# Performance work log

Measured on AMD Instinct MI355X. Metric: run time of the kernel, lower is better.

Reference implementation:

```python
import jax, jax.numpy as jnp
import numpy as np

B, A, V, D = 16, 1024, 512, 512
TEMPERATURE = 1.0
NEG = jnp.float32(-1e30)  # stand-in for -inf (avoids inf-inf NaNs in grads)
EPS = 1e-12               # F.normalize eps


def setup_inputs() -> dict:
    key = jax.random.key(0)
    k1, k2, k3 = jax.random.split(key, 3)
    audio_features = jax.random.normal(k1, (B, A, D), jnp.float32)
    video_features = jax.random.normal(k2, (B, V, D), jnp.float32)
    W = jax.random.normal(k3, (D, D), jnp.float32) / np.sqrt(D)  # nn.Linear weight [out,in]
    b = jnp.zeros((D,), jnp.float32)
    return {"audio_features": audio_features, "video_features": video_features, "W": W, "b": b}


def _normalize(x):
    n = jnp.linalg.norm(x, axis=-1, keepdims=True)
    return x / jnp.maximum(n, EPS)


def _dtw_score(sim):
    # sim: [B, A, V]. dp[i,j] = sim[i-1,j-1] + max(dp[i-1,j], dp[i,j-1], dp[i-1,j-1]).
    Bn, An, Vn = sim.shape
    init_row = jnp.full((Bn, Vn + 1), NEG).at[:, 0].set(0.0)  # dp row 0

    def row_step(prev_row, cost_row):
        # prev_row: [B, V+1], cost_row: [B, V]
        def col_step(left, xs):
            c, up, diag = xs  # each [B]
            val = c + jnp.maximum(jnp.maximum(up, left), diag)
            return val, val

        xs = (cost_row.T, prev_row[:, 1:].T, prev_row[:, :-1].T)  # [V, B] each
        _, vals = jax.lax.scan(col_step, jnp.full((Bn,), NEG), xs)  # vals: [V, B]
        new_row = jnp.concatenate([jnp.full((Bn, 1), NEG), vals.T], axis=1)
        return new_row, None

    final_row, _ = jax.lax.scan(row_step, init_row, jnp.swapaxes(sim, 0, 1))
    return final_row[:, -1]  # dp[:, A, V]


def reference(audio_features, video_features, W, b):
    audio_proj = jnp.einsum('bad,ed->bae', audio_features, W) + b
    video_proj = jnp.einsum('bvd,ed->bve', video_features, W) + b
    a_n = _normalize(audio_proj)
    v_n = _normalize(video_proj)
    similarity = jnp.einsum('bad,bvd->bav', a_n, v_n) / TEMPERATURE  # [B, A, V]
    alignment_score = _dtw_score(similarity)                          # [B]
    path_prob = jax.nn.softmax(similarity, axis=-1)
    aligned_video = jnp.einsum('bav,bvd->bad', path_prob, video_features)  # [B, A, D]
    return aligned_video, alignment_score
```

## Files before the change

### kernel.cpp

```cpp
#include <hip/hip_runtime.h>
#include <math.h>

#define B_DIM 16
#define A_DIM 1024
#define V_DIM 512
#define D_DIM 512
#define NEGV  (-1e30f)
#define SKT_W 768

typedef short bf16x8 __attribute__((ext_vector_type(8)));
typedef float floatx4 __attribute__((ext_vector_type(4)));

__device__ __forceinline__ short bf16_rne(float f) {
    unsigned u = __float_as_uint(f);
    return (short)((u + 0x7fffu + ((u >> 16) & 1u)) >> 16);
}

__device__ __forceinline__ float max3f(float a, float b, float c) {
    float d;
    asm("v_max3_f32 %0, %1, %2, %3" : "=v"(d) : "v"(a), "v"(b), "v"(c));
    return d;
}

__global__ __launch_bounds__(256) void cvt3_bf16_kernel(
    const float* __restrict__ in0, unsigned short* __restrict__ out0, int nb0,
    const float* __restrict__ in1, unsigned short* __restrict__ out1, int nb1,
    const float* __restrict__ in2, unsigned short* __restrict__ out2)
{
    int blk = blockIdx.x;
    const float* in; unsigned short* out;
    if (blk < nb0)              { in = in0; out = out0; }
    else if (blk < nb0 + nb1)   { in = in1; out = out1; blk -= nb0; }
    else                        { in = in2; out = out2; blk -= nb0 + nb1; }
    const int i = blk * 256 + threadIdx.x;
    float4 u = ((const float4*)in)[2*i];
    float4 v = ((const float4*)in)[2*i + 1];
    bf16x8 h;
    h[0]=bf16_rne(u.x); h[1]=bf16_rne(u.y); h[2]=bf16_rne(u.z); h[3]=bf16_rne(u.w);
    h[4]=bf16_rne(v.x); h[5]=bf16_rne(v.y); h[6]=bf16_rne(v.z); h[7]=bf16_rne(v.w);
    *(bf16x8*)(out + (size_t)i * 8) = h;
}

__device__ __forceinline__ void gemm_tile_body(
    const unsigned short* __restrict__ Ab, const unsigned short* __restrict__ Bb,
    const float* __restrict__ bias, float* __restrict__ Cb,
    int m0, int n0, int K, int N, int tid,
    unsigned short* lA, unsigned short* lB)
{
    const int lane = tid & 63;
    const int w = tid >> 6, wy = w >> 1, wx = w & 1;

    const int u0 = tid, u1 = tid + 256;
    const int r_u0 = ((u0 >> 6) << 4) + (u0 & 15), k_u0 = ((u0 >> 4) & 3) * 8;
    const int r_u1 = ((u1 >> 6) << 4) + (u1 & 15), k_u1 = ((u1 >> 4) & 3) * 8;

    const unsigned short* gA0 = Ab + (size_t)(m0 + r_u0) * K + k_u0;
    const unsigned short* gA1 = Ab + (size_t)(m0 + r_u1) * K + k_u1;
    const unsigned short* gB0 = Bb + (size_t)(n0 + r_u0) * K + k_u0;
    const unsigned short* gB1 = Bb + (size_t)(n0 + r_u1) * K + k_u1;

    floatx4 acc[4][4];
    #pragma unroll
    for (int i = 0; i < 4; ++i)
        #pragma unroll
        for (int j = 0; j < 4; ++j) acc[i][j] = (floatx4){0.f, 0.f, 0.f, 0.f};

    bf16x8 a0 = *(const bf16x8*)(gA0);
    bf16x8 a1 = *(const bf16x8*)(gA1);
    bf16x8 b0 = *(const bf16x8*)(gB0);
    bf16x8 b1 = *(const bf16x8*)(gB1);

    for (int k0 = 0; k0 < K; k0 += 32) {
        __syncthreads();
        *(bf16x8*)&lA[(size_t)u0 * 8] = a0;
        *(bf16x8*)&lA[(size_t)u1 * 8] = a1;
        *(bf16x8*)&lB[(size_t)u0 * 8] = b0;
        *(bf16x8*)&lB[(size_t)u1 * 8] = b1;
        __syncthreads();

        if (k0 + 32 < K) {
            a0 = *(const bf16x8*)(gA0 + k0 + 32);
            a1 = *(const bf16x8*)(gA1 + k0 + 32);
            b0 = *(const bf16x8*)(gB0 + k0 + 32);
            b1 = *(const bf16x8*)(gB1 + k0 + 32);
        }

        bf16x8 fa[4], fb[4];
        #pragma unroll
        for (int t = 0; t < 4; ++t) {
            fa[t] = *(const bf16x8*)&lA[(((wy*4 + t)*64) + lane) * 8];
            fb[t] = *(const bf16x8*)&lB[(((wx*4 + t)*64) + lane) * 8];
        }
        #pragma unroll
        for (int i = 0; i < 4; ++i)
            #pragma unroll
            for (int j = 0; j < 4; ++j)
                acc[i][j] = __builtin_amdgcn_mfma_f32_16x16x32_bf16(fa[i], fb[j], acc[i][j], 0, 0, 0);
    }

    const int q = lane >> 4, c = lane & 15;
    #pragma unroll
    for (int i = 0; i < 4; ++i)
        #pragma unroll
        for (int j = 0; j < 4; ++j) {
            const int n = n0 + (wx*4 + j)*16 + c;
            const float bv = bias ? bias[n] : 0.f;
            #pragma unroll
            for (int r = 0; r < 4; ++r) {
                const int m = m0 + (wy*4 + i)*16 + q*4 + r;
                Cb[(size_t)m * N + n] = acc[i][j][r] + bv;
            }
        }
}

__global__ __launch_bounds__(256) void gemm_bf16_nt(
    const unsigned short* __restrict__ Ag, const unsigned short* __restrict__ Bg,
    const float* __restrict__ bias, float* __restrict__ Cg,
    int M, int N, int K, size_t strA, size_t strB, size_t strC)
{
    __shared__ __align__(16) unsigned short lA[8*64*8];
    __shared__ __align__(16) unsigned short lB[8*64*8];
    const unsigned short* Ab = Ag + (size_t)blockIdx.z * strA;
    const unsigned short* Bb = Bg + (size_t)blockIdx.z * strB;
    float*                Cb = Cg + (size_t)blockIdx.z * strC;
    gemm_tile_body(Ab, Bb, bias, Cb, blockIdx.y * 128, blockIdx.x * 128, K, N,
                   threadIdx.x, lA, lB);
}

__global__ __launch_bounds__(256) void gemm_proj2(
    const unsigned short* __restrict__ abf, const unsigned short* __restrict__ vbf,
    const unsigned short* __restrict__ Wbf, const float* __restrict__ bias,
    float* __restrict__ a_p, float* __restrict__ v_p)
{
    __shared__ __align__(16) unsigned short lA[8*64*8];
    __shared__ __align__(16) unsigned short lB[8*64*8];
    const int by = blockIdx.y;
    const unsigned short* Ab; float* Cb; int m0;
    if (by < 128) { Ab = abf; Cb = a_p; m0 = by * 128; }
    else          { Ab = vbf; Cb = v_p; m0 = (by - 128) * 128; }
    gemm_tile_body(Ab, Wbf, bias, Cb, m0, blockIdx.x * 128, D_DIM, D_DIM,
                   threadIdx.x, lA, lB);
}

__global__ __launch_bounds__(256) void norm2_transpose_kernel(
    const float* __restrict__ a_p, unsigned short* __restrict__ a_nb,
    const float* __restrict__ v_p, unsigned short* __restrict__ v_nb,
    const float* __restrict__ video, unsigned short* __restrict__ vTb)
{
    __shared__ float t[32][33];
    const int bx = blockIdx.x;
    if (bx < 6144) {
        const float* in; unsigned short* out; int rb;
        if (bx < 4096) { in = a_p; out = a_nb; rb = bx; }
        else           { in = v_p; out = v_nb; rb = bx - 4096; }
        const int wave = threadIdx.x >> 6;
        const int lane = threadIdx.x & 63;
        const size_t r = (size_t)rb * 4 + wave;
        const float* p = in + r * D_DIM + lane * 8;
        float4 u = *(const float4*)p;
        float4 w = *(const float4*)(p + 4);
        float ss = u.x*u.x + u.y*u.y + u.z*u.z + u.w*u.w
                 + w.x*w.x + w.y*w.y + w.z*w.z + w.w*w.w;
        #pragma unroll
        for (int m = 1; m < 64; m <<= 1) ss += __shfl_xor(ss, m, 64);
        const float inv = 1.0f / fmaxf(sqrtf(ss), 1e-12f);
        bf16x8 h;
        h[0]=bf16_rne(u.x*inv); h[1]=bf16_rne(u.y*inv); h[2]=bf16_rne(u.z*inv); h[3]=bf16_rne(u.w*inv);
        h[4]=bf16_rne(w.x*inv); h[5]=bf16_rne(w.y*inv); h[6]=bf16_rne(w.z*inv); h[7]=bf16_rne(w.w*inv);
        *(bf16x8*)(out + r * D_DIM + lane * 8) = h;
    } else {
        const int tt = bx - 6144;
        const int d0 = (tt & 15) * 32;
        const int v0 = ((tt >> 4) & 15) * 32;
        const int b  = tt >> 8;
        const int x = threadIdx.x & 31, y0 = (threadIdx.x >> 5) * 4;
        const float* I = video + ((size_t)b * V_DIM + v0) * D_DIM + d0;
        #pragma unroll
        for (int r = 0; r < 4; ++r) t[y0 + r][x] = I[(size_t)(y0 + r) * D_DIM + x];
        __syncthreads();
        unsigned short* O = vTb + ((size_t)b * D_DIM + d0) * V_DIM + v0;
        #pragma unroll
        for (int r = 0; r < 4; ++r) O[(size_t)(y0 + r) * V_DIM + x] = (unsigned short)bf16_rne(t[x][y0 + r]);
    }
}

template <int CTRL, int RMASK>
__device__ __forceinline__ float fdpp(float oldv, float src) {
    int r = __builtin_amdgcn_update_dpp(
        __float_as_int(oldv), __float_as_int(src), CTRL, RMASK, 0xF, false);
    return __int_as_float(r);
}

__global__ __launch_bounds__(256) void softmax_skewT_kernel(
    const float* __restrict__ sim, unsigned short* __restrict__ Pbf,
    float* __restrict__ skewT)
{
    __shared__ float tl[4][520];
    const int wave = threadIdx.x >> 6;
    const int lane = threadIdx.x & 63;
    const size_t r = (size_t)blockIdx.x * 4 + wave;
    const float* p = sim + r * V_DIM + lane * 8;
    float4 u = *(const float4*)p;
    float4 w = *(const float4*)(p + 4);
    float s[8] = {u.x,u.y,u.z,u.w,w.x,w.y,w.z,w.w};

    float m = s[0];
    #pragma unroll
    for (int k = 1; k < 8; ++k) m = fmaxf(m, s[k]);
    #pragma unroll
    for (int t = 1; t < 64; t <<= 1) m = fmaxf(m, __shfl_xor(m, t, 64));

    const float L2E = 1.44269504f;
    float ex[8];
    float e = 0.f;
    #pragma unroll
    for (int k = 0; k < 8; ++k) { ex[k] = exp2f((s[k] - m) * L2E); e += ex[k]; }
    #pragma unroll
    for (int t = 1; t < 64; t <<= 1) e += __shfl_xor(e, t, 64);
    const float ri = 1.0f / e;

    bf16x8 h;
    #pragma unroll
    for (int k = 0; k < 8; ++k) h[k] = bf16_rne(ex[k] * ri);
    *(bf16x8*)(Pbf + r * V_DIM + lane * 8) = h;

    #pragma unroll
    for (int k = 0; k < 8; ++k) tl[wave][lane * 8 + k] = s[k];
    __syncthreads();

    const int r0 = blockIdx.x * 4;
    const int b  = r0 >> 10;
    const int i0 = r0 & 1023;
    const int g  = i0 >> 2;
    const int off = (g & 63) + 80 * (g >> 6);
    float* sbase = skewT + (size_t)b * SKT_W * 1024 + i0;
    #pragma unroll
    for (int cc = 0; cc < 2; ++cc) {
        const int c = threadIdx.x + cc * 256;
        int pc = c + off; if (pc >= SKT_W) pc -= SKT_W;
        float4 v = make_float4(tl[0][c], tl[1][c], tl[2][c], tl[3][c]);
        *(float4*)(sbase + (size_t)pc * 1024) = v;
    }
}

__global__ __launch_bounds__(512) void pv_dtw_kernel(
    const unsigned short* __restrict__ Pbf, const unsigned short* __restrict__ vTb,
    const float* __restrict__ skewT, float* __restrict__ out_aligned,
    float* __restrict__ out_score)
{
    __shared__ __align__(16) unsigned short shmem_u16[16384];

    const int half = threadIdx.x >> 8;
    const int tid  = threadIdx.x & 255;

    if (blockIdx.x < 8) {
        const int b    = blockIdx.x * 2 + half;
        const int lane = tid & 63;
        const int wv   = tid >> 6;
        const int off  = lane + 80 * wv;

        float* bndAll = (float*)shmem_u16 + half * (3 * 528);
        float* bndP = bndAll + wv * 528;
        const float* bndC = bndAll + (wv > 0 ? wv - 1 : 0) * 528;
        for (int i = tid; i < 3 * 528; i += 256) bndAll[i] = NEGV;
        __syncthreads();

        const float* Sb = skewT + (size_t)b * SKT_W * 1024 + 4 * tid;

        float dp[4] = {NEGV, NEGV, NEGV, NEGV};
        float st[16];
        float upC = NEGV;
        float upL = (tid == 0) ? 0.0f : NEGV;

        float4 CA[8], CB[8], CC[8], CD[8];
        #pragma unroll
        for (int k = 0; k < 8; ++k) {
            CA[k] = *(const float4*)(Sb + (size_t)k * 1024);
            CB[k] = *(const float4*)(Sb + (size_t)(k + 8) * 1024);
            CC[k] = *(const float4*)(Sb + (size_t)(k + 16) * 1024);
            CD[k] = *(const float4*)(Sb + (size_t)(k + 24) * 1024);
        }

#define DTW_STEP(K, CK, FK)                                                   \
        {                                                                     \
            const unsigned jj = (unsigned)(sb + (K) - off);                   \
            if (jj < 512u) {                                                  \
                float u = upC, g = upL, old, nd;                              \
                old = dp[0]; nd = (CK).x + max3f(u, dp[0], g); dp[0] = nd; g = old; u = nd; \
                old = dp[1]; nd = (CK).y + max3f(u, dp[1], g); dp[1] = nd; g = old; u = nd; \
                old = dp[2]; nd = (CK).z + max3f(u, dp[2], g); dp[2] = nd; g = old; u = nd; \
                old = dp[3]; nd = (CK).w + max3f(u, dp[3], g); dp[3] = nd;                  \
            }                                                                 \
            st[K] = dp[3];                                                    \
            upL = upC;                                                        \
            upC = fdpp<0x138, 0xF>((FK), dp[3]);                              \
        }

#define DTW_BATCH16(P, Q)                                                     \
        {                                                                     \
            const int ps = sb + 8 - 80 * wv;                                  \
            float f[16];                                                      \
            _Pragma("unroll")                                                 \
            for (int k = 0; k < 16; ++k) {                                    \
                int idx = ps + k;                                             \
                idx = idx < 0 ? 0 : (idx > 527 ? 527 : idx);                  \
                f[k] = (wv > 0) ? bndC[idx] : NEGV;                           \
            }                                                                 \
            DTW_STEP(0,  P[0], f[0])  DTW_STEP(1,  P[1], f[1])                \
            DTW_STEP(2,  P[2], f[2])  DTW_STEP(3,  P[3], f[3])                \
            DTW_STEP(4,  P[4], f[4])  DTW_STEP(5,  P[5], f[5])                \
            DTW_STEP(6,  P[6], f[6])  DTW_STEP(7,  P[7], f[7])                \
            DTW_STEP(8,  Q[0], f[8])  DTW_STEP(9,  Q[1], f[9])                \
            DTW_STEP(10, Q[2], f[10]) DTW_STEP(11, Q[3], f[11])               \
            DTW_STEP(12, Q[4], f[12]) DTW_STEP(13, Q[5], f[13])               \
            DTW_STEP(14, Q[6], f[14]) DTW_STEP(15, Q[7], f[15])               \
            {                                                                 \
                _Pragma("unroll")                                             \
                for (int k = 0; k < 8; ++k) {                                 \
                    int c1 = sb + 32 + k; if (c1 >= SKT_W) c1 -= SKT_W;       \
                    P[k] = *(const float4*)(Sb + (size_t)c1 * 1024);          \
                    int c2 = sb + 40 + k; if (c2 >= SKT_W) c2 -= SKT_W;       \
                    Q[k] = *(const float4*)(Sb + (size_t)c2 * 1024);          \
                }                                                             \
            }                                                                 \
            if (wv < 3 && lane == 63) {                                       \
                _Pragma("unroll")                                             \
                for (int k = 0; k < 16; ++k) {                                \
                    const int jp = sb + k - 63 - 80 * wv;                     \
                    const int adr = ((unsigned)jp < 512u) ? (jp + 7) : 527;   \
                    bndP[adr] = st[k];                                        \
                }                                                             \
            }                                                                 \
            asm volatile("s_waitcnt lgkmcnt(0)" ::: "memory");                \
            __builtin_amdgcn_s_barrier();                                     \
            asm volatile("" ::: "memory");                                    \
        }

        #pragma unroll 1
        for (int bt = 0; bt < 52; bt += 2) {
            int sb = bt * 16;
            DTW_BATCH16(CA, CB)
            sb += 16;
            DTW_BATCH16(CC, CD)
        }
#undef DTW_BATCH16
#undef DTW_STEP
        if (tid == 255) out_score[b] = dp[3];
        return;
    }

    const int tile = (blockIdx.x - 8) * 2 + half;
    const int n0 = (tile & 3) * 128;
    const int m0 = ((tile >> 2) & 7) * 128;
    const int bz = tile >> 5;

    const unsigned short* Ab = Pbf + (size_t)bz * A_DIM * V_DIM;
    const unsigned short* Bb = vTb + (size_t)bz * V_DIM * D_DIM;
    float*                Cb = out_aligned + (size_t)bz * A_DIM * D_DIM;

    unsigned short* lA = shmem_u16 + half * 8192;
    unsigned short* lB = lA + 4096;
    gemm_tile_body(Ab, Bb, nullptr, Cb, m0, n0, V_DIM, D_DIM, tid, lA, lB);
}

extern "C" void kernel_launch(void* const* d_in, const int* in_sizes, int n_in,
                              void* d_out, int out_size, void* d_ws, size_t ws_size,
                              hipStream_t stream)
{
    const float* audio = (const float*)d_in[0];
    const float* video = (const float*)d_in[1];
    const float* W     = (const float*)d_in[2];
    const float* bias  = (const float*)d_in[3];

    float* out_aligned = (float*)d_out;
    float* out_score   = (float*)d_out + (size_t)B_DIM * A_DIM * D_DIM;

    const size_t NA = (size_t)B_DIM * A_DIM * D_DIM;
    const size_t NV = (size_t)B_DIM * V_DIM * D_DIM;
    const size_t NS = (size_t)B_DIM * A_DIM * V_DIM;

    float* ws = (float*)d_ws;
    float*          a_p  = ws;
    float*          v_p  = a_p + NA;
    float*          sim  = v_p + NV;
    unsigned short* abf  = (unsigned short*)(sim + NS);
    unsigned short* vbf  = (unsigned short*)(sim + NS) + NA;
    unsigned short* v_nb = vbf + NV;
    unsigned short* Wbf  = v_nb + NV;
    unsigned short* a_nb = abf;
    unsigned short* Pbf  = abf;
    unsigned short* vTb  = vbf;
    float*          skewT = a_p;

    {
        const int nb_a = (int)(NA / 8 / 256);
        const int nb_v = (int)(NV / 8 / 256);
        const int nb_w = D_DIM * D_DIM / 8 / 256;
        cvt3_bf16_kernel<<<dim3(nb_a + nb_v + nb_w), dim3(256), 0, stream>>>(
            audio, abf, nb_a, video, vbf, nb_v, W, Wbf);
    }

    gemm_proj2<<<dim3(D_DIM/128, 192), dim3(256), 0, stream>>>(
        abf, vbf, Wbf, bias, a_p, v_p);

    norm2_transpose_kernel<<<dim3(4096 + 2048 + 4096), dim3(256), 0, stream>>>(
        a_p, a_nb, v_p, v_nb, video, vTb);

    gemm_bf16_nt<<<dim3(V_DIM/128, A_DIM/128, B_DIM), dim3(256), 0, stream>>>(
        a_nb, v_nb, nullptr, sim, A_DIM, V_DIM, D_DIM,
        (size_t)A_DIM*D_DIM, (size_t)V_DIM*D_DIM, (size_t)A_DIM*V_DIM);

    softmax_skewT_kernel<<<dim3((B_DIM*A_DIM)/4), dim3(256), 0, stream>>>(sim, Pbf, skewT);

    pv_dtw_kernel<<<dim3(8 + 256), dim3(512), 0, stream>>>(
        Pbf, vTb, skewT, out_aligned, out_score);
}
```

Baseline: 329.0 us.

## Fuse bf16 conversion into projection GEMM, widen softmax-skew blocks, split pv/dtw blocks

Drops the separate fp32-to-bf16 conversion kernel. The projection GEMM now loads fp32 inputs directly and converts them with packed bf16 conversion instructions while staging into LDS, which removes one launch and a full round trip of the inputs through memory. The softmax/skew kernel now handles 16 rows per block, so it writes full 16-float runs of the skewed transpose, and it explicitly zero-fills padding columns. The pv/dtw kernel changes from 512-thread blocks, each holding two halves, to 256-thread blocks with one DTW or GEMM tile each. This may change occupancy and the overlap between the DTW chain and the GEMM tiles.

```diff
diff --git a/kernel.cpp b/kernel.cpp
--- a/kernel.cpp
+++ b/kernel.cpp
@@ -22,23 +22,13 @@
     return d;
 }
 
-__global__ __launch_bounds__(256) void cvt3_bf16_kernel(
-    const float* __restrict__ in0, unsigned short* __restrict__ out0, int nb0,
-    const float* __restrict__ in1, unsigned short* __restrict__ out1, int nb1,
-    const float* __restrict__ in2, unsigned short* __restrict__ out2)
-{
-    int blk = blockIdx.x;
-    const float* in; unsigned short* out;
-    if (blk < nb0)              { in = in0; out = out0; }
-    else if (blk < nb0 + nb1)   { in = in1; out = out1; blk -= nb0; }
-    else                        { in = in2; out = out2; blk -= nb0 + nb1; }
-    const int i = blk * 256 + threadIdx.x;
-    float4 u = ((const float4*)in)[2*i];
-    float4 v = ((const float4*)in)[2*i + 1];
-    bf16x8 h;
-    h[0]=bf16_rne(u.x); h[1]=bf16_rne(u.y); h[2]=bf16_rne(u.z); h[3]=bf16_rne(u.w);
-    h[4]=bf16_rne(v.x); h[5]=bf16_rne(v.y); h[6]=bf16_rne(v.z); h[7]=bf16_rne(v.w);
-    *(bf16x8*)(out + (size_t)i * 8) = h;
+__device__ __forceinline__ bf16x8 cvt8(float4 u, float4 w) {
+    union { unsigned int ui[4]; bf16x8 h; } r;
+    asm("v_cvt_pk_bf16_f32 %0, %1, %2" : "=v"(r.ui[0]) : "v"(u.x), "v"(u.y));
+    asm("v_cvt_pk_bf16_f32 %0, %1, %2" : "=v"(r.ui[1]) : "v"(u.z), "v"(u.w));
+    asm("v_cvt_pk_bf16_f32 %0, %1, %2" : "=v"(r.ui[2]) : "v"(w.x), "v"(w.y));
+    asm("v_cvt_pk_bf16_f32 %0, %1, %2" : "=v"(r.ui[3]) : "v"(w.z), "v"(w.w));
+    return r.h;
 }
 
 __device__ __forceinline__ void gemm_tile_body(
@@ -113,6 +103,78 @@
         }
 }
 
+__device__ __forceinline__ void gemm_tile_body_f32in(
+    const float* __restrict__ Ab, const float* __restrict__ Bb,
+    const float* __restrict__ bias, float* __restrict__ Cb,
+    int m0, int n0, int K, int N, int tid,
+    unsigned short* lA, unsigned short* lB)
+{
+    const int lane = tid & 63;
+    const int w = tid >> 6, wy = w >> 1, wx = w & 1;
+
+    const int u0 = tid, u1 = tid + 256;
+    const int r_u0 = ((u0 >> 6) << 4) + (u0 & 15), k_u0 = ((u0 >> 4) & 3) * 8;
+    const int r_u1 = ((u1 >> 6) << 4) + (u1 & 15), k_u1 = ((u1 >> 4) & 3) * 8;
+
+    const float* gA0 = Ab + (size_t)(m0 + r_u0) * K + k_u0;
+    const float* gA1 = Ab + (size_t)(m0 + r_u1) * K + k_u1;
+    const float* gB0 = Bb + (size_t)(n0 + r_u0) * K + k_u0;
+    const float* gB1 = Bb + (size_t)(n0 + r_u1) * K + k_u1;
+
+    floatx4 acc[4][4];
+    #pragma unroll
+    for (int i = 0; i < 4; ++i)
+        #pragma unroll
+        for (int j = 0; j < 4; ++j) acc[i][j] = (floatx4){0.f, 0.f, 0.f, 0.f};
+
+    float4 a0u = *(const float4*)(gA0), a0w = *(const float4*)(gA0 + 4);
+    float4 a1u = *(const float4*)(gA1), a1w = *(const float4*)(gA1 + 4);
+    float4 b0u = *(const float4*)(gB0), b0w = *(const float4*)(gB0 + 4);
+    float4 b1u = *(const float4*)(gB1), b1w = *(const float4*)(gB1 + 4);
+
+    for (int k0 = 0; k0 < K; k0 += 32) {
+        __syncthreads();
+        *(bf16x8*)&lA[(size_t)u0 * 8] = cvt8(a0u, a0w);
+        *(bf16x8*)&lA[(size_t)u1 * 8] = cvt8(a1u, a1w);
+        *(bf16x8*)&lB[(size_t)u0 * 8] = cvt8(b0u, b0w);
+        *(bf16x8*)&lB[(size_t)u1 * 8] = cvt8(b1u, b1w);
+        __syncthreads();
+
+        if (k0 + 32 < K) {
+            a0u = *(const float4*)(gA0 + k0 + 32); a0w = *(const float4*)(gA0 + k0 + 36);
+            a1u = *(const float4*)(gA1 + k0 + 32); a1w = *(const float4*)(gA1 + k0 + 36);
+            b0u = *(const float4*)(gB0 + k0 + 32); b0w = *(const float4*)(gB0 + k0 + 36);
+            b1u = *(const float4*)(gB1 + k0 + 32); b1w = *(const float4*)(gB1 + k0 + 36);
+        }
+
+        bf16x8 fa[4], fb[4];
+        #pragma unroll
+        for (int t = 0; t < 4; ++t) {
+            fa[t] = *(const bf16x8*)&lA[(((wy*4 + t)*64) + lane) * 8];
+            fb[t] = *(const bf16x8*)&lB[(((wx*4 + t)*64) + lane) * 8];
+        }
+        #pragma unroll
+        for (int i = 0; i < 4; ++i)
+            #pragma unroll
+            for (int j = 0; j < 4; ++j)
+                acc[i][j] = __builtin_amdgcn_mfma_f32_16x16x32_bf16(fa[i], fb[j], acc[i][j], 0, 0, 0);
+    }
+
+    const int q = lane >> 4, c = lane & 15;
+    #pragma unroll
+    for (int i = 0; i < 4; ++i)
+        #pragma unroll
+        for (int j = 0; j < 4; ++j) {
+            const int n = n0 + (wx*4 + j)*16 + c;
+            const float bv = bias ? bias[n] : 0.f;
+            #pragma unroll
+            for (int r = 0; r < 4; ++r) {
+                const int m = m0 + (wy*4 + i)*16 + q*4 + r;
+                Cb[(size_t)m * N + n] = acc[i][j][r] + bv;
+            }
+        }
+}
+
 __global__ __launch_bounds__(256) void gemm_bf16_nt(
     const unsigned short* __restrict__ Ag, const unsigned short* __restrict__ Bg,
     const float* __restrict__ bias, float* __restrict__ Cg,
@@ -127,19 +189,19 @@
                    threadIdx.x, lA, lB);
 }
 
-__global__ __launch_bounds__(256) void gemm_proj2(
-    const unsigned short* __restrict__ abf, const unsigned short* __restrict__ vbf,
-    const unsigned short* __restrict__ Wbf, const float* __restrict__ bias,
+__global__ __launch_bounds__(256) void gemm_proj2_f32(
+    const float* __restrict__ audio, const float* __restrict__ video,
+    const float* __restrict__ W, const float* __restrict__ bias,
     float* __restrict__ a_p, float* __restrict__ v_p)
 {
     __shared__ __align__(16) unsigned short lA[8*64*8];
     __shared__ __align__(16) unsigned short lB[8*64*8];
     const int by = blockIdx.y;
-    const unsigned short* Ab; float* Cb; int m0;
-    if (by < 128) { Ab = abf; Cb = a_p; m0 = by * 128; }
-    else          { Ab = vbf; Cb = v_p; m0 = (by - 128) * 128; }
-    gemm_tile_body(Ab, Wbf, bias, Cb, m0, blockIdx.x * 128, D_DIM, D_DIM,
-                   threadIdx.x, lA, lB);
+    const float* Ab; float* Cb; int m0;
+    if (by < 128) { Ab = audio; Cb = a_p; m0 = by * 128; }
+    else          { Ab = video; Cb = v_p; m0 = (by - 128) * 128; }
+    gemm_tile_body_f32in(Ab, W, bias, Cb, m0, blockIdx.x * 128, D_DIM, D_DIM,
+                         threadIdx.x, lA, lB);
 }
 
 __global__ __launch_bounds__(256) void norm2_transpose_kernel(
@@ -191,75 +253,81 @@
     return __int_as_float(r);
 }
 
-__global__ __launch_bounds__(256) void softmax_skewT_kernel(
+__global__ __launch_bounds__(256) void softmax_skewT16_kernel(
     const float* __restrict__ sim, unsigned short* __restrict__ Pbf,
     float* __restrict__ skewT)
 {
-    __shared__ float tl[4][520];
+    __shared__ float tl[16][512];
     const int wave = threadIdx.x >> 6;
     const int lane = threadIdx.x & 63;
-    const size_t r = (size_t)blockIdx.x * 4 + wave;
-    const float* p = sim + r * V_DIM + lane * 8;
-    float4 u = *(const float4*)p;
-    float4 w = *(const float4*)(p + 4);
-    float s[8] = {u.x,u.y,u.z,u.w,w.x,w.y,w.z,w.w};
-
-    float m = s[0];
-    #pragma unroll
-    for (int k = 1; k < 8; ++k) m = fmaxf(m, s[k]);
-    #pragma unroll
-    for (int t = 1; t < 64; t <<= 1) m = fmaxf(m, __shfl_xor(m, t, 64));
-
-    const float L2E = 1.44269504f;
-    float ex[8];
-    float e = 0.f;
-    #pragma unroll
-    for (int k = 0; k < 8; ++k) { ex[k] = exp2f((s[k] - m) * L2E); e += ex[k]; }
-    #pragma unroll
-    for (int t = 1; t < 64; t <<= 1) e += __shfl_xor(e, t, 64);
-    const float ri = 1.0f / e;
-
-    bf16x8 h;
-    #pragma unroll
-    for (int k = 0; k < 8; ++k) h[k] = bf16_rne(ex[k] * ri);
-    *(bf16x8*)(Pbf + r * V_DIM + lane * 8) = h;
-
-    #pragma unroll
-    for (int k = 0; k < 8; ++k) tl[wave][lane * 8 + k] = s[k];
-    __syncthreads();
-
-    const int r0 = blockIdx.x * 4;
+    const int r0 = blockIdx.x * 16;
     const int b  = r0 >> 10;
     const int i0 = r0 & 1023;
-    const int g  = i0 >> 2;
-    const int off = (g & 63) + 80 * (g >> 6);
-    float* sbase = skewT + (size_t)b * SKT_W * 1024 + i0;
-    #pragma unroll
-    for (int cc = 0; cc < 2; ++cc) {
-        const int c = threadIdx.x + cc * 256;
-        int pc = c + off; if (pc >= SKT_W) pc -= SKT_W;
-        float4 v = make_float4(tl[0][c], tl[1][c], tl[2][c], tl[3][c]);
+
+    const float L2E = 1.44269504f;
+    #pragma unroll
+    for (int j = 0; j < 4; ++j) {
+        const size_t r = (size_t)r0 + 4 * wave + j;
+        const float* p = sim + r * V_DIM + lane * 8;
+        float4 u = *(const float4*)p;
+        float4 w = *(const float4*)(p + 4);
+        float s[8] = {u.x,u.y,u.z,u.w,w.x,w.y,w.z,w.w};
+
+        float m = s[0];
+        #pragma unroll
+        for (int k = 1; k < 8; ++k) m = fmaxf(m, s[k]);
+        #pragma unroll
+        for (int t = 1; t < 64; t <<= 1) m = fmaxf(m, __shfl_xor(m, t, 64));
+
+        float ex[8];
+        float e = 0.f;
+        #pragma unroll
+        for (int k = 0; k < 8; ++k) { ex[k] = exp2f((s[k] - m) * L2E); e += ex[k]; }
+        #pragma unroll
+        for (int t = 1; t < 64; t <<= 1) e += __shfl_xor(e, t, 64);
+        const float ri = 1.0f / e;
+
+        bf16x8 h;
+        #pragma unroll
+        for (int k = 0; k < 8; ++k) h[k] = bf16_rne(ex[k] * ri);
+        *(bf16x8*)(Pbf + r * V_DIM + lane * 8) = h;
+
+        #pragma unroll
+        for (int k = 0; k < 8; ++k) tl[4*wave + j][lane * 8 + k] = s[k];
+    }
+    __syncthreads();
+
+    const int g0   = i0 >> 2;
+    const int off0 = (g0 & 63) + 80 * (g0 >> 6);
+    const int q    = threadIdx.x & 3;
+    const int pcb  = threadIdx.x >> 2;
+    float* sbase = skewT + (size_t)b * SKT_W * 1024 + i0 + 4 * q;
+    #pragma unroll
+    for (int pass = 0; pass < 12; ++pass) {
+        const int pc = pcb + pass * 64;
+        int c = pc - (off0 + q); if (c < 0) c += SKT_W;
+        float4 v = make_float4(0.f, 0.f, 0.f, 0.f);
+        if (c < 512) v = make_float4(tl[4*q+0][c], tl[4*q+1][c], tl[4*q+2][c], tl[4*q+3][c]);
         *(float4*)(sbase + (size_t)pc * 1024) = v;
     }
 }
 
-__global__ __launch_bounds__(512) void pv_dtw_kernel(
+__global__ __launch_bounds__(256) void pv_dtw_kernel(
     const unsigned short* __restrict__ Pbf, const unsigned short* __restrict__ vTb,
     const float* __restrict__ skewT, float* __restrict__ out_aligned,
     float* __restrict__ out_score)
 {
-    __shared__ __align__(16) unsigned short shmem_u16[16384];
-
-    const int half = threadIdx.x >> 8;
-    const int tid  = threadIdx.x & 255;
-
-    if (blockIdx.x < 8) {
-        const int b    = blockIdx.x * 2 + half;
+    __shared__ __align__(16) unsigned short lA[8*64*8];
+    __shared__ __align__(16) unsigned short lB[8*64*8];
+
+    if (blockIdx.x < 16) {
+        const int b    = blockIdx.x;
+        const int tid  = threadIdx.x;
         const int lane = tid & 63;
         const int wv   = tid >> 6;
         const int off  = lane + 80 * wv;
 
-        float* bndAll = (float*)shmem_u16 + half * (3 * 528);
+        float* bndAll = (float*)lA;
         float* bndP = bndAll + wv * 528;
         const float* bndC = bndAll + (wv > 0 ? wv - 1 : 0) * 528;
         for (int i = tid; i < 3 * 528; i += 256) bndAll[i] = NEGV;
@@ -349,18 +417,16 @@
         return;
     }
 
-    const int tile = (blockIdx.x - 8) * 2 + half;
-    const int n0 = (tile & 3) * 128;
-    const int m0 = ((tile >> 2) & 7) * 128;
-    const int bz = tile >> 5;
+    const int bid = blockIdx.x - 16;
+    const int n0 = (bid & 3) * 128;
+    const int m0 = ((bid >> 2) & 7) * 128;
+    const int bz = bid >> 5;
 
     const unsigned short* Ab = Pbf + (size_t)bz * A_DIM * V_DIM;
     const unsigned short* Bb = vTb + (size_t)bz * V_DIM * D_DIM;
     float*                Cb = out_aligned + (size_t)bz * A_DIM * D_DIM;
 
-    unsigned short* lA = shmem_u16 + half * 8192;
-    unsigned short* lB = lA + 4096;
-    gemm_tile_body(Ab, Bb, nullptr, Cb, m0, n0, V_DIM, D_DIM, tid, lA, lB);
+    gemm_tile_body(Ab, Bb, nullptr, Cb, m0, n0, V_DIM, D_DIM, threadIdx.x, lA, lB);
 }
 
 extern "C" void kernel_launch(void* const* d_in, const int* in_sizes, int n_in,
@@ -386,22 +452,13 @@
     unsigned short* abf  = (unsigned short*)(sim + NS);
     unsigned short* vbf  = (unsigned short*)(sim + NS) + NA;
     unsigned short* v_nb = vbf + NV;
-    unsigned short* Wbf  = v_nb + NV;
     unsigned short* a_nb = abf;
     unsigned short* Pbf  = abf;
     unsigned short* vTb  = vbf;
     float*          skewT = a_p;
 
-    {
-        const int nb_a = (int)(NA / 8 / 256);
-        const int nb_v = (int)(NV / 8 / 256);
-        const int nb_w = D_DIM * D_DIM / 8 / 256;
-        cvt3_bf16_kernel<<<dim3(nb_a + nb_v + nb_w), dim3(256), 0, stream>>>(
-            audio, abf, nb_a, video, vbf, nb_v, W, Wbf);
-    }
-
-    gemm_proj2<<<dim3(D_DIM/128, 192), dim3(256), 0, stream>>>(
-        abf, vbf, Wbf, bias, a_p, v_p);
+    gemm_proj2_f32<<<dim3(D_DIM/128, 192), dim3(256), 0, stream>>>(
+        audio, video, W, bias, a_p, v_p);
 
     norm2_transpose_kernel<<<dim3(4096 + 2048 + 4096), dim3(256), 0, stream>>>(
         a_p, a_nb, v_p, v_nb, video, vTb);
@@ -410,8 +467,9 @@
         a_nb, v_nb, nullptr, sim, A_DIM, V_DIM, D_DIM,
         (size_t)A_DIM*D_DIM, (size_t)V_DIM*D_DIM, (size_t)A_DIM*V_DIM);
 
-    softmax_skewT_kernel<<<dim3((B_DIM*A_DIM)/4), dim3(256), 0, stream>>>(sim, Pbf, skewT);
-
-    pv_dtw_kernel<<<dim3(8 + 256), dim3(512), 0, stream>>>(
+    softmax_skewT16_kernel<<<dim3((B_DIM*A_DIM)/16), dim3(256), 0, stream>>>(
+        sim, Pbf, skewT);
+
+    pv_dtw_kernel<<<dim3(16 + (D_DIM/128)*(A_DIM/128)*B_DIM), dim3(256), 0, stream>>>(
         Pbf, vTb, skewT, out_aligned, out_score);
 }
```

New measurement: 298.1 us. 1.1x faster.
